# Performance work log

Measured on AMD Instinct MI355X. Metric: run time of the kernel, lower is better.

The kernel has to match this reference:

```python
import jax, jax.numpy as jnp
import numpy as np
from jax import lax

WINDOW = 11
SIGMA = 1.5
K1 = 0.01
K2 = 0.03
DATA_RANGE = 1.0


def _gaussian_kernel(channels):
    coords = jnp.arange(WINDOW, dtype=jnp.float32) - (WINDOW // 2)
    g = jnp.exp(-(coords ** 2) / (2.0 * SIGMA ** 2))
    g = g / g.sum()
    k2d = g[:, None] * g[None, :]                      # [W, W]
    # depthwise kernel, OIHW with I=1, O=channels (feature_group_count=channels)
    return jnp.broadcast_to(k2d, (channels, 1, WINDOW, WINDOW))


def _depthwise_blur(img, kernel, channels):
    pad = WINDOW // 2
    return lax.conv_general_dilated(
        img, kernel,
        window_strides=(1, 1),
        padding=[(pad, pad), (pad, pad)],
        dimension_numbers=('NCHW', 'OIHW', 'NCHW'),
        feature_group_count=channels,
    )


def setup_inputs() -> dict:
    key = jax.random.key(0)
    kx, ky = jax.random.split(key)
    shape = (16, 3, 512, 512)
    x = jax.random.uniform(kx, shape, dtype=jnp.float32)
    y = jax.random.uniform(ky, shape, dtype=jnp.float32)
    return {"x": x, "y": y}


def reference(x, y):
    channels = x.shape[1]
    kernel = _gaussian_kernel(channels)

    mu_x = _depthwise_blur(x, kernel, channels)
    mu_y = _depthwise_blur(y, kernel, channels)
    mu_x_sq = mu_x * mu_x
    mu_y_sq = mu_y * mu_y
    mu_xy = mu_x * mu_y

    sigma_x_sq = _depthwise_blur(x * x, kernel, channels) - mu_x_sq
    sigma_y_sq = _depthwise_blur(y * y, kernel, channels) - mu_y_sq
    sigma_xy = _depthwise_blur(x * y, kernel, channels) - mu_xy

    C1 = (K1 * DATA_RANGE) ** 2
    C2 = (K2 * DATA_RANGE) ** 2
    numerator = (2.0 * mu_xy + C1) * (2.0 * sigma_xy + C2)
    denominator = (mu_x_sq + mu_y_sq + C1) * (sigma_x_sq + sigma_y_sq + C2)
    ssim_map = numerator / (denominator + 1e-8)
    return 1.0 - ssim_map.mean()
```

## Files before the change

### kernel.cpp

```cpp
#include <hip/hip_runtime.h>
#include <cmath>

#define WIN 11
#define HALO 5
#define IMG 512
#define NIMG 48
#define TS 64
#define HR (TS + 2*HALO)
#define NTILE (IMG/TS)
#define NBLK (NIMG*NTILE*NTILE)
#define NPIX (16.0 * 3.0 * 512.0 * 512.0)

typedef _Float16 f16;
typedef _Float16 h2 __attribute__((ext_vector_type(2)));

struct GaussW { unsigned hw[WIN]; };

__device__ __forceinline__ unsigned pk2(float a, float b) {
    auto h = __builtin_amdgcn_cvt_pkrtz(a, b);
    return __builtin_bit_cast(unsigned, h);
}
__device__ __forceinline__ h2 uph(unsigned u) {
    return __builtin_bit_cast(h2, u);
}
__device__ __forceinline__ unsigned dnh(h2 v) {
    return __builtin_bit_cast(unsigned, v);
}

__global__ void __launch_bounds__(64) zero_kernel(float* out) {
    if (threadIdx.x == 0) out[0] = 0.f;
}

__global__ void __launch_bounds__(64) finish_kernel(float* out) {
    if (threadIdx.x == 0)
        out[0] = 1.0f - out[0] * (float)(1.0 / NPIX);
}

template<int USE_ATOMIC>
__global__ void __launch_bounds__(1024, 8) fused_ssim(
        const float* __restrict__ xin, const float* __restrict__ yin,
        float* __restrict__ outp, GaussW W) {
    __shared__ uint4 hb[HR][32];
    __shared__ float wsum[16];
    const int tid = threadIdx.x;
    const int tx = blockIdx.x, ty = blockIdx.y;
    const size_t ibase = (size_t)blockIdx.z * (size_t)(IMG * IMG);
    const float* __restrict__ xb = xin + ibase;
    const float* __restrict__ yb = yin + ibase;

    const int cg  = tid & 15;
    const int rr  = tid >> 4;
    const int gx0 = tx * TS + cg * 4 - HALO;
    const bool cint = (gx0 >= 0) && (gx0 + 13 < IMG);

    #pragma unroll
    for (int it = 0; it < 2; ++it) {
        const int r = it * 64 + rr;
        if (r < HR) {
            const int gy = ty * TS - HALO + r;
            if ((unsigned)gy < IMG) {
                const float* xr = xb + (size_t)gy * IMG;
                const float* yr = yb + (size_t)gy * IMG;
                float xv[14], yv[14];
                if (cint) {
                    xv[0] = xr[gx0];  yv[0] = yr[gx0];
                    #pragma unroll
                    for (int q = 0; q < 3; ++q) {
                        float4 a = *(const float4*)(xr + gx0 + 1 + 4*q);
                        float4 b = *(const float4*)(yr + gx0 + 1 + 4*q);
                        xv[1+4*q]=a.x; xv[2+4*q]=a.y; xv[3+4*q]=a.z; xv[4+4*q]=a.w;
                        yv[1+4*q]=b.x; yv[2+4*q]=b.y; yv[3+4*q]=b.z; yv[4+4*q]=b.w;
                    }
                    xv[13] = xr[gx0 + 13];  yv[13] = yr[gx0 + 13];
                } else {
                    #pragma unroll
                    for (int j = 0; j < 14; ++j) {
                        int gx = gx0 + j;
                        bool ok = ((unsigned)gx < IMG);
                        xv[j] = ok ? xr[gx] : 0.f;
                        yv[j] = ok ? yr[gx] : 0.f;
                    }
                }
                h2 a0[4], a1[4];
                #pragma unroll
                for (int o = 0; o < 4; ++o) {
                    a0[o] = (h2){(f16)0, (f16)0};
                    a1[o] = (h2){(f16)0, (f16)0};
                }
                #pragma unroll
                for (int j = 0; j < 14; ++j) {
                    float xs = xv[j], ys = yv[j];
                    float xy = xs * ys;
                    float ss = fmaf(xs, xs, ys * ys);
                    h2 c0 = uph(pk2(xs, ys));
                    h2 c1 = uph(pk2(ss, xy));
                    #pragma unroll
                    for (int o = 0; o < 4; ++o) {
                        int k = j - o;
                        if (k >= 0 && k < WIN) {
                            h2 wk = uph(W.hw[k]);
                            a0[o] += wk * c0;
                            a1[o] += wk * c1;
                        }
                    }
                }
                uint4 u0, u1;
                u0.x = dnh(a0[0]); u0.y = dnh(a1[0]);
                u0.z = dnh(a0[1]); u0.w = dnh(a1[1]);
                u1.x = dnh(a0[2]); u1.y = dnh(a1[2]);
                u1.z = dnh(a0[3]); u1.w = dnh(a1[3]);
                hb[r][cg]      = u0;
                hb[r][cg + 16] = u1;
            } else {
                uint4 z = make_uint4(0u, 0u, 0u, 0u);
                hb[r][cg]      = z;
                hb[r][cg + 16] = z;
            }
        }
    }
    __syncthreads();

    const int idx = tid & 31;
    const int rbase = (tid >> 5) * 2;

    h2 acc[2][4];
    #pragma unroll
    for (int o = 0; o < 2; ++o)
        #pragma unroll
        for (int f = 0; f < 4; ++f)
            acc[o][f] = (h2){(f16)0, (f16)0};

    #pragma unroll
    for (int j = 0; j < 12; ++j) {
        uint4 u = hb[rbase + j][idx];
        h2 f0 = uph(u.x), f1 = uph(u.y), f2 = uph(u.z), f3 = uph(u.w);
        #pragma unroll
        for (int o = 0; o < 2; ++o) {
            int k = j - o;
            if (k >= 0 && k < WIN) {
                h2 wk = uph(W.hw[k]);
                acc[o][0] += wk * f0;
                acc[o][1] += wk * f1;
                acc[o][2] += wk * f2;
                acc[o][3] += wk * f3;
            }
        }
    }

    const float C1 = 0.01f * 0.01f;
    const float C2 = 0.03f * 0.03f;
    float local = 0.f;
    #pragma unroll
    for (int o = 0; o < 2; ++o) {
        #pragma unroll
        for (int p = 0; p < 2; ++p) {
            h2 m  = acc[o][2*p];
            h2 se = acc[o][2*p+1];
            float mux = (float)m[0];
            float muy = (float)m[1];
            float es  = (float)se[0];
            float exy = (float)se[1];
            float mux2 = mux * mux, muy2 = muy * muy, muxy = mux * muy;
            float num = (2.f * muxy + C1) * (2.f * (exy - muxy) + C2);
            float den = (mux2 + muy2 + C1) * ((es - mux2 - muy2) + C2);
            local += num * __builtin_amdgcn_rcpf(den + 1e-8f);
        }
    }

    #pragma unroll
    for (int off = 32; off > 0; off >>= 1)
        local += __shfl_down(local, off, 64);
    if ((tid & 63) == 0) wsum[tid >> 6] = local;
    __syncthreads();
    if (tid == 0) {
        float bs = 0.f;
        #pragma unroll
        for (int wv = 0; wv < 16; ++wv) bs += wsum[wv];
        if (USE_ATOMIC) {
            atomicAdd(outp, bs);
        } else {
            int bid = (blockIdx.z * NTILE + blockIdx.y) * NTILE + blockIdx.x;
            outp[bid] = bs;
        }
    }
}

__global__ void __launch_bounds__(256) reduce_kernel(
        const float* __restrict__ partial, float* __restrict__ out) {
    __shared__ float wsum[4];
    const int tid = threadIdx.x;
    float s = 0.f;
    for (int i = tid; i < NBLK; i += 256) s += partial[i];
    #pragma unroll
    for (int off = 32; off > 0; off >>= 1)
        s += __shfl_down(s, off, 64);
    if ((tid & 63) == 0) wsum[tid >> 6] = s;
    __syncthreads();
    if (tid == 0)
        out[0] = 1.0f - (wsum[0] + wsum[1] + wsum[2] + wsum[3]) * (float)(1.0 / NPIX);
}

extern "C" void kernel_launch(void* const* d_in, const int* in_sizes, int n_in,
                              void* d_out, int out_size, void* d_ws, size_t ws_size,
                              hipStream_t stream) {
    const float* x = (const float*)d_in[0];
    const float* y = (const float*)d_in[1];
    float* out = (float*)d_out;

    double g[WIN], s = 0.0;
    for (int i = 0; i < WIN; ++i) {
        double d = (double)(i - WIN / 2);
        g[i] = exp(-(d * d) / (2.0 * 1.5 * 1.5));
        s += g[i];
    }
    float wf[WIN];
    for (int i = 0; i < WIN; ++i) wf[i] = (float)(g[i] / s);

    GaussW gw;
    _Float16 wh[WIN];
    double hsum = 0.0;
    for (int i = 0; i < WIN; ++i) { wh[i] = (_Float16)wf[i]; hsum += (double)(float)wh[i]; }
    wh[WIN/2] = (_Float16)((float)wh[WIN/2] + (float)(1.0 - hsum));
    for (int i = 0; i < WIN; ++i) {
        unsigned short b = __builtin_bit_cast(unsigned short, wh[i]);
        gw.hw[i] = (unsigned)b | ((unsigned)b << 16);
    }

    if (ws_size >= (size_t)NBLK * sizeof(float)) {
        float* partial = (float*)d_ws;
        hipLaunchKernelGGL((fused_ssim<0>), dim3(NTILE, NTILE, NIMG), dim3(1024),
                           0, stream, x, y, partial, gw);
        hipLaunchKernelGGL(reduce_kernel, dim3(1), dim3(256), 0, stream,
                           partial, out);
    } else {
        hipLaunchKernelGGL(zero_kernel, dim3(1), dim3(64), 0, stream, out);
        hipLaunchKernelGGL((fused_ssim<1>), dim3(NTILE, NTILE, NIMG), dim3(1024),
                           0, stream, x, y, out, gw);
        hipLaunchKernelGGL(finish_kernel, dim3(1), dim3(64), 0, stream, out);
    }
}
```

Before: 160.7 us.

## Make SSIM kernel persistent with register prefetch of next tile

Replaces the one-block-per-tile grid with 512 persistent blocks that each process six 64x64 tiles in sequence. Each block prefetches the next tile's input rows into registers while the vertical blur of the current tile runs, overlapping global loads with compute. Horizontal blur work per thread doubles to 8 outputs over 18 inputs, and the launch bound drops to 4 blocks per CU to leave room for the extra registers. The tradeoffs are fewer resident waves, added per-tile syncs, and a smaller partial-sum array to reduce.

```diff
diff --git a/kernel.cpp b/kernel.cpp
--- a/kernel.cpp
+++ b/kernel.cpp
@@ -8,7 +8,9 @@
 #define TS 64
 #define HR (TS + 2*HALO)
 #define NTILE (IMG/TS)
-#define NBLK (NIMG*NTILE*NTILE)
+#define NTT (NIMG*NTILE*NTILE)
+#define PBLK 512
+#define TPB (NTT/PBLK)
 #define NPIX (16.0 * 3.0 * 512.0 * 512.0)
 
 typedef _Float16 f16;
@@ -37,133 +39,147 @@
 }
 
 template<int USE_ATOMIC>
-__global__ void __launch_bounds__(1024, 8) fused_ssim(
+__global__ void __launch_bounds__(1024, 4) fused_ssim(
         const float* __restrict__ xin, const float* __restrict__ yin,
         float* __restrict__ outp, GaussW W) {
     __shared__ uint4 hb[HR][32];
     __shared__ float wsum[16];
     const int tid = threadIdx.x;
-    const int tx = blockIdx.x, ty = blockIdx.y;
-    const size_t ibase = (size_t)blockIdx.z * (size_t)(IMG * IMG);
-    const float* __restrict__ xb = xin + ibase;
-    const float* __restrict__ yb = yin + ibase;
-
-    const int cg  = tid & 15;
-    const int rr  = tid >> 4;
-    const int gx0 = tx * TS + cg * 4 - HALO;
-    const bool cint = (gx0 >= 0) && (gx0 + 13 < IMG);
-
-    #pragma unroll
-    for (int it = 0; it < 2; ++it) {
-        const int r = it * 64 + rr;
-        if (r < HR) {
-            const int gy = ty * TS - HALO + r;
-            if ((unsigned)gy < IMG) {
-                const float* xr = xb + (size_t)gy * IMG;
-                const float* yr = yb + (size_t)gy * IMG;
-                float xv[14], yv[14];
-                if (cint) {
-                    xv[0] = xr[gx0];  yv[0] = yr[gx0];
-                    #pragma unroll
-                    for (int q = 0; q < 3; ++q) {
-                        float4 a = *(const float4*)(xr + gx0 + 1 + 4*q);
-                        float4 b = *(const float4*)(yr + gx0 + 1 + 4*q);
-                        xv[1+4*q]=a.x; xv[2+4*q]=a.y; xv[3+4*q]=a.z; xv[4+4*q]=a.w;
-                        yv[1+4*q]=b.x; yv[2+4*q]=b.y; yv[3+4*q]=b.z; yv[4+4*q]=b.w;
-                    }
-                    xv[13] = xr[gx0 + 13];  yv[13] = yr[gx0 + 13];
-                } else {
-                    #pragma unroll
-                    for (int j = 0; j < 14; ++j) {
-                        int gx = gx0 + j;
-                        bool ok = ((unsigned)gx < IMG);
-                        xv[j] = ok ? xr[gx] : 0.f;
-                        yv[j] = ok ? yr[gx] : 0.f;
-                    }
+    const int cg = tid & 7;
+    const int r  = tid >> 3;
+    const int idx   = tid & 31;
+    const int rbase = (tid >> 5) * 2;
+
+    const int t0 = blockIdx.x * TPB;
+
+    float xv[18], yv[18];
+    float local = 0.f;
+
+    auto prefetch = [&](int t) {
+        if (r >= HR) return;
+        const int tg  = t0 + t;
+        const int img = tg >> 6;
+        const int rem = tg & 63;
+        const int ty  = rem >> 3;
+        const int tx  = rem & 7;
+        const float* xb = xin + (size_t)img * (IMG * IMG);
+        const float* yb = yin + (size_t)img * (IMG * IMG);
+        const int gy  = ty * TS - HALO + r;
+        const int gx0 = tx * TS + cg * 8 - HALO;
+        const bool rowok = ((unsigned)gy < IMG);
+        const float* xr = xb + (size_t)gy * IMG;
+        const float* yr = yb + (size_t)gy * IMG;
+        if (rowok && gx0 >= 0 && gx0 + 17 < IMG) {
+            xv[0] = xr[gx0];  yv[0] = yr[gx0];
+            #pragma unroll
+            for (int q = 0; q < 4; ++q) {
+                float4 a = *(const float4*)(xr + gx0 + 1 + 4*q);
+                float4 b = *(const float4*)(yr + gx0 + 1 + 4*q);
+                xv[1+4*q]=a.x; xv[2+4*q]=a.y; xv[3+4*q]=a.z; xv[4+4*q]=a.w;
+                yv[1+4*q]=b.x; yv[2+4*q]=b.y; yv[3+4*q]=b.z; yv[4+4*q]=b.w;
+            }
+            xv[17] = xr[gx0 + 17];  yv[17] = yr[gx0 + 17];
+        } else {
+            #pragma unroll
+            for (int j = 0; j < 18; ++j) {
+                int gx = gx0 + j;
+                bool ok = rowok && ((unsigned)gx < IMG);
+                xv[j] = ok ? xr[gx] : 0.f;
+                yv[j] = ok ? yr[gx] : 0.f;
+            }
+        }
+    };
+
+    auto hblur = [&]() {
+        if (r >= HR) return;
+        h2 a0[8], a1[8];
+        #pragma unroll
+        for (int o = 0; o < 8; ++o) {
+            a0[o] = (h2){(f16)0, (f16)0};
+            a1[o] = (h2){(f16)0, (f16)0};
+        }
+        #pragma unroll
+        for (int j = 0; j < 18; ++j) {
+            float xs = xv[j], ys = yv[j];
+            h2 c0 = uph(pk2(xs, ys));
+            h2 c1 = uph(pk2(fmaf(xs, xs, ys * ys), xs * ys));
+            #pragma unroll
+            for (int o = 0; o < 8; ++o) {
+                int k = j - o;
+                if (k >= 0 && k < WIN) {
+                    h2 wk = uph(W.hw[k]);
+                    a0[o] += wk * c0;
+                    a1[o] += wk * c1;
                 }
-                h2 a0[4], a1[4];
-                #pragma unroll
-                for (int o = 0; o < 4; ++o) {
-                    a0[o] = (h2){(f16)0, (f16)0};
-                    a1[o] = (h2){(f16)0, (f16)0};
+            }
+        }
+        #pragma unroll
+        for (int p = 0; p < 4; ++p) {
+            uint4 u;
+            u.x = dnh(a0[2*p]);     u.y = dnh(a1[2*p]);
+            u.z = dnh(a0[2*p + 1]); u.w = dnh(a1[2*p + 1]);
+            hb[r][cg + 8*p] = u;
+        }
+    };
+
+    auto phase2 = [&]() {
+        h2 acc[2][4];
+        #pragma unroll
+        for (int o = 0; o < 2; ++o)
+            #pragma unroll
+            for (int f = 0; f < 4; ++f)
+                acc[o][f] = (h2){(f16)0, (f16)0};
+        #pragma unroll
+        for (int j = 0; j < 12; ++j) {
+            uint4 u = hb[rbase + j][idx];
+            h2 f0 = uph(u.x), f1 = uph(u.y), f2 = uph(u.z), f3 = uph(u.w);
+            #pragma unroll
+            for (int o = 0; o < 2; ++o) {
+                int k = j - o;
+                if (k >= 0 && k < WIN) {
+                    h2 wk = uph(W.hw[k]);
+                    acc[o][0] += wk * f0;
+                    acc[o][1] += wk * f1;
+                    acc[o][2] += wk * f2;
+                    acc[o][3] += wk * f3;
                 }
-                #pragma unroll
-                for (int j = 0; j < 14; ++j) {
-                    float xs = xv[j], ys = yv[j];
-                    float xy = xs * ys;
-                    float ss = fmaf(xs, xs, ys * ys);
-                    h2 c0 = uph(pk2(xs, ys));
-                    h2 c1 = uph(pk2(ss, xy));
-                    #pragma unroll
-                    for (int o = 0; o < 4; ++o) {
-                        int k = j - o;
-                        if (k >= 0 && k < WIN) {
-                            h2 wk = uph(W.hw[k]);
-                            a0[o] += wk * c0;
-                            a1[o] += wk * c1;
-                        }
-                    }
-                }
-                uint4 u0, u1;
-                u0.x = dnh(a0[0]); u0.y = dnh(a1[0]);
-                u0.z = dnh(a0[1]); u0.w = dnh(a1[1]);
-                u1.x = dnh(a0[2]); u1.y = dnh(a1[2]);
-                u1.z = dnh(a0[3]); u1.w = dnh(a1[3]);
-                hb[r][cg]      = u0;
-                hb[r][cg + 16] = u1;
-            } else {
-                uint4 z = make_uint4(0u, 0u, 0u, 0u);
-                hb[r][cg]      = z;
-                hb[r][cg + 16] = z;
-            }
-        }
-    }
+            }
+        }
+        const float C1 = 0.01f * 0.01f;
+        const float C2 = 0.03f * 0.03f;
+        #pragma unroll
+        for (int o = 0; o < 2; ++o) {
+            #pragma unroll
+            for (int p = 0; p < 2; ++p) {
+                h2 m  = acc[o][2*p];
+                h2 se = acc[o][2*p + 1];
+                float mux = (float)m[0];
+                float muy = (float)m[1];
+                float es  = (float)se[0];
+                float exy = (float)se[1];
+                float mux2 = mux*mux, muy2 = muy*muy, muxy = mux*muy;
+                float num = (2.f*muxy + C1) * (2.f*(exy - muxy) + C2);
+                float den = (mux2 + muy2 + C1) * ((es - mux2 - muy2) + C2);
+                local += num * __builtin_amdgcn_rcpf(den + 1e-8f);
+            }
+        }
+    };
+
+    prefetch(0);
+    hblur();
+    prefetch(1);
     __syncthreads();
 
-    const int idx = tid & 31;
-    const int rbase = (tid >> 5) * 2;
-
-    h2 acc[2][4];
-    #pragma unroll
-    for (int o = 0; o < 2; ++o)
-        #pragma unroll
-        for (int f = 0; f < 4; ++f)
-            acc[o][f] = (h2){(f16)0, (f16)0};
-
-    #pragma unroll
-    for (int j = 0; j < 12; ++j) {
-        uint4 u = hb[rbase + j][idx];
-        h2 f0 = uph(u.x), f1 = uph(u.y), f2 = uph(u.z), f3 = uph(u.w);
-        #pragma unroll
-        for (int o = 0; o < 2; ++o) {
-            int k = j - o;
-            if (k >= 0 && k < WIN) {
-                h2 wk = uph(W.hw[k]);
-                acc[o][0] += wk * f0;
-                acc[o][1] += wk * f1;
-                acc[o][2] += wk * f2;
-                acc[o][3] += wk * f3;
-            }
-        }
-    }
-
-    const float C1 = 0.01f * 0.01f;
-    const float C2 = 0.03f * 0.03f;
-    float local = 0.f;
-    #pragma unroll
-    for (int o = 0; o < 2; ++o) {
-        #pragma unroll
-        for (int p = 0; p < 2; ++p) {
-            h2 m  = acc[o][2*p];
-            h2 se = acc[o][2*p+1];
-            float mux = (float)m[0];
-            float muy = (float)m[1];
-            float es  = (float)se[0];
-            float exy = (float)se[1];
-            float mux2 = mux * mux, muy2 = muy * muy, muxy = mux * muy;
-            float num = (2.f * muxy + C1) * (2.f * (exy - muxy) + C2);
-            float den = (mux2 + muy2 + C1) * ((es - mux2 - muy2) + C2);
-            local += num * __builtin_amdgcn_rcpf(den + 1e-8f);
+    for (int t = 0; t < TPB; ++t) {
+        phase2();
+        if (t + 1 < TPB) {
+            __syncthreads();
+            hblur();
+            if (t + 2 < TPB) {
+                prefetch(t + 2);
+                __builtin_amdgcn_sched_barrier(0);
+            }
+            __syncthreads();
         }
     }
 
@@ -179,8 +195,7 @@
         if (USE_ATOMIC) {
             atomicAdd(outp, bs);
         } else {
-            int bid = (blockIdx.z * NTILE + blockIdx.y) * NTILE + blockIdx.x;
-            outp[bid] = bs;
+            outp[blockIdx.x] = bs;
         }
     }
 }
@@ -190,7 +205,7 @@
     __shared__ float wsum[4];
     const int tid = threadIdx.x;
     float s = 0.f;
-    for (int i = tid; i < NBLK; i += 256) s += partial[i];
+    for (int i = tid; i < PBLK; i += 256) s += partial[i];
     #pragma unroll
     for (int off = 32; off > 0; off >>= 1)
         s += __shfl_down(s, off, 64);
@@ -226,15 +241,15 @@
         gw.hw[i] = (unsigned)b | ((unsigned)b << 16);
     }
 
-    if (ws_size >= (size_t)NBLK * sizeof(float)) {
+    if (ws_size >= (size_t)PBLK * sizeof(float)) {
         float* partial = (float*)d_ws;
-        hipLaunchKernelGGL((fused_ssim<0>), dim3(NTILE, NTILE, NIMG), dim3(1024),
+        hipLaunchKernelGGL((fused_ssim<0>), dim3(PBLK), dim3(1024),
                            0, stream, x, y, partial, gw);
         hipLaunchKernelGGL(reduce_kernel, dim3(1), dim3(256), 0, stream,
                            partial, out);
     } else {
         hipLaunchKernelGGL(zero_kernel, dim3(1), dim3(64), 0, stream, out);
-        hipLaunchKernelGGL((fused_ssim<1>), dim3(NTILE, NTILE, NIMG), dim3(1024),
+        hipLaunchKernelGGL((fused_ssim<1>), dim3(PBLK), dim3(1024),
                            0, stream, x, y, out, gw);
         hipLaunchKernelGGL(finish_kernel, dim3(1), dim3(64), 0, stream, out);
     }
```

Result: faster. 149.5 us (-6.9%).
